# Performance work log

Measured on AMD Instinct MI355X. Metric: run time of the kernel, lower is better.

Reference implementation:

```python
import jax, jax.numpy as jnp
import numpy as np

D = 512
H = 8
HD = D // H
EPS = 1e-6


def layer_norm(x, a, b):
    # torch: std is unbiased (ddof=1); note division by (std + eps), not sqrt(var+eps)
    mean = x.mean(-1, keepdims=True)
    std = jnp.sqrt(x.var(-1, ddof=1, keepdims=True))
    return a * (x - mean) / (std + EPS) + b


def setup_inputs() -> dict:
    key = jax.random.key(0)
    ks = jax.random.split(key, 8)
    x = jax.random.normal(ks[0], (4, 2048, D), dtype=jnp.float32)
    s = 0.02
    return {
        "x": x,
        "ln1_a": jnp.ones((D,), jnp.float32),
        "ln1_b": jnp.zeros((D,), jnp.float32),
        "ln2_a": jnp.ones((D,), jnp.float32),
        "ln2_b": jnp.zeros((D,), jnp.float32),
        "wq": jax.random.normal(ks[1], (D, D), jnp.float32) * s,  # [out, in] torch layout
        "wk": jax.random.normal(ks[2], (D, D), jnp.float32) * s,
        "wv": jax.random.normal(ks[3], (D, D), jnp.float32) * s,
        "wo": jax.random.normal(ks[4], (D, D), jnp.float32) * s,
        "w1": jax.random.normal(ks[5], (D, D), jnp.float32) * s,  # MLP hidden == dim
        "b1": jnp.zeros((D,), jnp.float32),
        "w2": jax.random.normal(ks[6], (D, D), jnp.float32) * s,
        "b2": jnp.zeros((D,), jnp.float32),
    }


def reference(x, ln1_a, ln1_b, ln2_a, ln2_b, wq, wk, wv, wo, w1, b1, w2, b2):
    B, S, _ = x.shape
    xn = layer_norm(x, ln1_a, ln1_b)
    # attention (non-causal, dropout=identity in eval)
    q = (xn @ wq.T).reshape(B, S, H, HD)
    k = (xn @ wk.T).reshape(B, S, H, HD)
    v = (xn @ wv.T).reshape(B, S, H, HD)
    scores = jnp.einsum("bshd,bthd->bhst", q, k) / jnp.sqrt(jnp.float32(HD))
    probs = jax.nn.softmax(scores.astype(jnp.float32), axis=-1).astype(q.dtype)
    attn = jnp.einsum("bhst,bthd->bshd", probs, v).reshape(B, S, D)
    h = xn + attn @ wo.T
    # MLP
    hn = layer_norm(h, ln2_a, ln2_b)
    ffn = jax.nn.relu(hn @ w1.T + b1) @ w2.T + b2
    return h + ffn
```

## Files before the change

### kernel.cpp

```cpp
#include <hip/hip_runtime.h>


typedef short s16x8 __attribute__((ext_vector_type(8)));
typedef float f32x4 __attribute__((ext_vector_type(4)));
typedef unsigned short u16;
typedef u16 u16x4 __attribute__((ext_vector_type(4)));

__device__ __forceinline__ u16 f2b(float f) {
  union { float f; unsigned u; } c; c.f = f;
  return (u16)((c.u + 0x7FFFu + ((c.u >> 16) & 1u)) >> 16);
}

__device__ __forceinline__ f32x4 mfma16(s16x8 a, s16x8 b, f32x4 c) {
  return __builtin_amdgcn_mfma_f32_16x16x32_bf16(a, b, c, 0, 0, 0);
}

__device__ __forceinline__ void gload_lds16(const u16* g, u16* l) {
  __builtin_amdgcn_global_load_lds(
      (const __attribute__((address_space(1))) unsigned*)g,
      (__attribute__((address_space(3))) unsigned*)l, 16, 0, 0);
}

__global__ __launch_bounds__(256) void cast_w(
    const float* __restrict__ s0, const float* __restrict__ s1,
    const float* __restrict__ s2, const float* __restrict__ s3,
    const float* __restrict__ s4, const float* __restrict__ s5,
    u16* __restrict__ dst)
{
  int i = blockIdx.x * 256 + threadIdx.x;
  const float* s;
  switch (blockIdx.y) {
    case 0: s = s0; break; case 1: s = s1; break; case 2: s = s2; break;
    case 3: s = s3; break; case 4: s = s4; break; default: s = s5; break;
  }
  float4 v = ((const float4*)s)[i];
  u16x4 o; o.x = f2b(v.x); o.y = f2b(v.y); o.z = f2b(v.z); o.w = f2b(v.w);
  *(u16x4*)(dst + (size_t)blockIdx.y * 262144 + (size_t)i * 4) = o;
}

template<int OF, int OB>
__global__ __launch_bounds__(256) void ln_kernel(
    const float* __restrict__ x, const float* __restrict__ ga,
    const float* __restrict__ gbv, float* __restrict__ yf, u16* __restrict__ yb)
{
  int row = blockIdx.x * 4 + (threadIdx.x >> 6);
  int lane = threadIdx.x & 63;
  size_t base = (size_t)row * 512 + lane * 8;
  const float4* xr = (const float4*)(x + base);
  float4 v0 = xr[0], v1 = xr[1];
  float s  = v0.x + v0.y + v0.z + v0.w + v1.x + v1.y + v1.z + v1.w;
  float ss = v0.x*v0.x + v0.y*v0.y + v0.z*v0.z + v0.w*v0.w
           + v1.x*v1.x + v1.y*v1.y + v1.z*v1.z + v1.w*v1.w;
  #pragma unroll
  for (int m = 1; m < 64; m <<= 1) { s += __shfl_xor(s, m); ss += __shfl_xor(ss, m); }
  float mean = s * (1.0f / 512.0f);
  float var  = fmaxf((ss - 512.0f * mean * mean) * (1.0f / 511.0f), 0.0f);
  float inv  = 1.0f / (sqrtf(var) + 1e-6f);
  const float4* ap = (const float4*)(ga + lane * 8);
  const float4* bp = (const float4*)(gbv + lane * 8);
  float4 a0 = ap[0], a1 = ap[1], b0 = bp[0], b1 = bp[1];
  float4 y0, y1;
  y0.x = (v0.x-mean)*inv*a0.x + b0.x;  y0.y = (v0.y-mean)*inv*a0.y + b0.y;
  y0.z = (v0.z-mean)*inv*a0.z + b0.z;  y0.w = (v0.w-mean)*inv*a0.w + b0.w;
  y1.x = (v1.x-mean)*inv*a1.x + b1.x;  y1.y = (v1.y-mean)*inv*a1.y + b1.y;
  y1.z = (v1.z-mean)*inv*a1.z + b1.z;  y1.w = (v1.w-mean)*inv*a1.w + b1.w;
  if (OF) { float4* o = (float4*)(yf + base); o[0] = y0; o[1] = y1; }
  if (OB) {
    union { s16x8 v; u16 u[8]; } pk;
    pk.u[0]=f2b(y0.x); pk.u[1]=f2b(y0.y); pk.u[2]=f2b(y0.z); pk.u[3]=f2b(y0.w);
    pk.u[4]=f2b(y1.x); pk.u[5]=f2b(y1.y); pk.u[6]=f2b(y1.z); pk.u[7]=f2b(y1.w);
    *(s16x8*)(yb + base) = pk.v;
  }
}

template<int MODE>
__global__ __launch_bounds__(256) void gemm128(
    const u16* __restrict__ A, const u16* __restrict__ W,
    const float* __restrict__ bias, const float* __restrict__ resid,
    float* __restrict__ outf, u16* __restrict__ outb,
    u16* __restrict__ outb2, u16* __restrict__ outb3, float qscale)
{
  __shared__ u16 als[2][128 * 32];
  __shared__ u16 bls[2][128 * 32];
  int t = threadIdx.x, lane = t & 63, w = t >> 6;
  int l15 = lane & 15, g = lane >> 4;
  int wr = w >> 1, wc = w & 1;
  int mbase = blockIdx.x * 128, nbase = blockIdx.y * 128;

  int r0 = t >> 2, cs = (t & 3) ^ ((r0 >> 1) & 3);
  size_t offA0 = (size_t)(mbase + r0) * 512 + cs * 8;
  size_t offA1 = (size_t)(mbase + r0 + 64) * 512 + cs * 8;
  size_t offB0 = (size_t)(nbase + r0) * 512 + cs * 8;
  size_t offB1 = (size_t)(nbase + r0 + 64) * 512 + cs * 8;

  #define GSTAGE(buf, k0) do {                                    \
    gload_lds16(A + (k0) + offA0, &als[buf][(w * 64) * 8]);       \
    gload_lds16(A + (k0) + offA1, &als[buf][(256 + w * 64) * 8]); \
    gload_lds16(W + (k0) + offB0, &bls[buf][(w * 64) * 8]);       \
    gload_lds16(W + (k0) + offB1, &bls[buf][(256 + w * 64) * 8]); \
  } while (0)

  int ar[4], br[4];
  #pragma unroll
  for (int i = 0; i < 4; ++i) {
    int rA = wr * 64 + i * 16 + l15;
    ar[i] = rA * 32 + ((g ^ ((rA >> 1) & 3)) << 3);
    int rB = wc * 64 + i * 16 + l15;
    br[i] = rB * 32 + ((g ^ ((rB >> 1) & 3)) << 3);
  }

  f32x4 zero = {0.0f, 0.0f, 0.0f, 0.0f};
  f32x4 acc[4][4];
  #pragma unroll
  for (int mi = 0; mi < 4; ++mi)
    #pragma unroll
    for (int ni = 0; ni < 4; ++ni) acc[mi][ni] = zero;

  GSTAGE(0, 0);
  __syncthreads();
  int cur = 0;
  for (int kk = 0; kk < 16; ++kk) {
    if (kk < 15) GSTAGE(cur ^ 1, (kk + 1) * 32);
    s16x8 af[4], bfr[4];
    #pragma unroll
    for (int i = 0; i < 4; ++i) {
      af[i]  = *(const s16x8*)&als[cur][ar[i]];
      bfr[i] = *(const s16x8*)&bls[cur][br[i]];
    }
    #pragma unroll
    for (int mi = 0; mi < 4; ++mi)
      #pragma unroll
      for (int ni = 0; ni < 4; ++ni)
        acc[mi][ni] = mfma16(af[mi], bfr[ni], acc[mi][ni]);
    __syncthreads();
    cur ^= 1;
  }
  #undef GSTAGE

  #pragma unroll
  for (int ni = 0; ni < 4; ++ni) {
    int n = nbase + wc * 64 + ni * 16 + l15;
    float bv = (MODE & 1) ? bias[n] : 0.0f;
    #pragma unroll
    for (int mi = 0; mi < 4; ++mi) {
      #pragma unroll
      for (int r = 0; r < 4; ++r) {
        int m = mbase + wr * 64 + mi * 16 + 4 * g + r;
        float v = acc[mi][ni][r] + bv;
        if (MODE & 2) v = fmaxf(v, 0.0f);
        if (MODE & 4) v += resid[(size_t)m * 512 + n];
        if (MODE & 8) outf[(size_t)m * 512 + n] = v;
        if (MODE & 16) outb[(size_t)m * 512 + n] = f2b(v);
        if (MODE & 64) {
          if (nbase < 512) {
            outb[(size_t)m * 512 + n] = f2b(v * qscale);
          } else if (nbase < 1024) {
            outb2[(size_t)m * 512 + (n - 512)] = f2b(v);
          } else {
            int nn = n - 1024;
            int sidx = m & 2047;
            int jj = sidx & 31, lo4 = jj & 15, b5 = jj >> 4;
            int pos = ((lo4 >> 2) << 3) + ((lo4 & 3) << 1) + b5;
            outb3[(size_t)((m >> 11) * 512 + nn) * 2048 + (sidx & ~31) + pos] = f2b(v);
          }
        }
      }
    }
  }
}

__global__ __launch_bounds__(256) void attn_kernel(
    const u16* __restrict__ q, const u16* __restrict__ k,
    const u16* __restrict__ vt, u16* __restrict__ o)
{
  __shared__ u16 kls[2][64 * 64];
  __shared__ u16 vls[2][64 * 64];
  int t = threadIdx.x, lane = t & 63, w = t >> 6;
  int l15 = lane & 15, g = lane >> 4;
  int sw = l15 & 7;
  int lrow = lane >> 3;
  int lchunk = (lane & 7) ^ (lrow & 7);
  int fid = blockIdx.x + 32 * blockIdx.y;
  int xcd = fid & 7, rest = fid >> 3;
  int bh = xcd * 4 + (rest & 3);
  int qt = rest >> 2;
  int bb = bh >> 3, h = bh & 7;
  int qbase = qt * 64 + w * 16;

  const u16* qp = q + (size_t)(bb * 2048 + qbase + l15) * 512 + h * 64 + g * 8;
  s16x8 qf0 = *(const s16x8*)qp;
  s16x8 qf1 = *(const s16x8*)(qp + 32);
  f32x4 zero = {0.0f, 0.0f, 0.0f, 0.0f};
  f32x4 oacc[4] = {zero, zero, zero, zero};
  float lsum = 0.0f;
  const u16* kb0 = k + (size_t)(bb * 2048) * 512 + h * 64;
  const u16* vb0 = vt + (size_t)((bb * 8 + h) * 64) * 2048;

  #define STAGE(nb, tt) do {                                                  \
    int r0 = w * 16 + lrow;                                                   \
    const u16* ks0 = kb0 + (size_t)((tt) * 64 + r0) * 512 + lchunk * 8;       \
    const u16* vs0 = vb0 + (size_t)r0 * 2048 + (tt) * 64 + lchunk * 8;        \
    gload_lds16(ks0, &kls[nb][(w * 16) * 64]);                                \
    gload_lds16(ks0 + (size_t)8 * 512, &kls[nb][(w * 16 + 8) * 64]);          \
    gload_lds16(vs0, &vls[nb][(w * 16) * 64]);                                \
    gload_lds16(vs0 + (size_t)8 * 2048, &vls[nb][(w * 16 + 8) * 64]);         \
  } while (0)

  STAGE(0, 0);
  __syncthreads();
  int cur = 0;

  for (int kt = 0; kt < 32; ++kt) {
    if (kt + 1 < 32) STAGE(cur ^ 1, kt + 1);
    f32x4 s[4];
    #pragma unroll
    for (int kg = 0; kg < 4; ++kg) {
      int rb = (kg * 16 + l15) * 64;
      s16x8 ka = *(const s16x8*)&kls[cur][rb + ((g ^ sw) << 3)];
      s16x8 kc = *(const s16x8*)&kls[cur][rb + (((4 + g) ^ sw) << 3)];
      s[kg] = mfma16(ka, qf0, zero);
      s[kg] = mfma16(kc, qf1, s[kg]);
    }
    union { s16x8 v8; unsigned u32v[4]; } pk[2];
    #pragma unroll
    for (int b2 = 0; b2 < 2; ++b2) {
      #pragma unroll
      for (int r = 0; r < 4; ++r) {
        float p0 = __builtin_amdgcn_exp2f(s[2 * b2][r]);
        float p1 = __builtin_amdgcn_exp2f(s[2 * b2 + 1][r]);
        lsum += p0 + p1;
        union { float f; unsigned u; } a, b;
        a.f = p0; b.f = p1;
        pk[b2].u32v[r] = (a.u >> 16) | (b.u & 0xffff0000u);
      }
    }
    #pragma unroll
    for (int b2 = 0; b2 < 2; ++b2) {
      #pragma unroll
      for (int nf = 0; nf < 4; ++nf) {
        s16x8 vf = *(const s16x8*)
            &vls[cur][(nf * 16 + l15) * 64 + ((((b2 << 2) | g) ^ sw) << 3)];
        oacc[nf] = mfma16(pk[b2].v8, vf, oacc[nf]);
      }
    }
    __syncthreads();
    cur ^= 1;
  }
  #undef STAGE

  lsum += __shfl_xor(lsum, 16);
  lsum += __shfl_xor(lsum, 32);
  float linv = 1.0f / lsum;
  size_t obase = (size_t)(bb * 2048 + qbase + 4 * g) * 512 + h * 64 + l15;
  #pragma unroll
  for (int r = 0; r < 4; ++r) {
    float lr = __shfl(linv, 4 * g + r);
    #pragma unroll
    for (int nf = 0; nf < 4; ++nf)
      o[obase + (size_t)r * 512 + nf * 16] = f2b(oacc[nf][r] * lr);
  }
}

extern "C" void kernel_launch(void* const* d_in, const int* in_sizes, int n_in,
                              void* d_out, int out_size, void* d_ws, size_t ws_size,
                              hipStream_t stream)
{
  const float* x     = (const float*)d_in[0];
  const float* ln1_a = (const float*)d_in[1];
  const float* ln1_b = (const float*)d_in[2];
  const float* ln2_a = (const float*)d_in[3];
  const float* ln2_b = (const float*)d_in[4];
  const float* wq = (const float*)d_in[5];
  const float* wk = (const float*)d_in[6];
  const float* wv = (const float*)d_in[7];
  const float* wo = (const float*)d_in[8];
  const float* w1 = (const float*)d_in[9];
  const float* b1 = (const float*)d_in[10];
  const float* w2 = (const float*)d_in[11];
  const float* b2 = (const float*)d_in[12];

  char* ws = (char*)d_ws;
  float* xn_f = (float*)(ws + (size_t)0);
  float* h_f  = (float*)(ws + ((size_t)16 << 20));
  u16* xn_b = (u16*)(ws + ((size_t)32 << 20));
  u16* q_b  = (u16*)(ws + ((size_t)40 << 20));
  u16* k_b  = (u16*)(ws + ((size_t)48 << 20));
  u16* vt_b = (u16*)(ws + ((size_t)56 << 20));
  u16* at_b = (u16*)(ws + ((size_t)64 << 20));
  u16* wb   = (u16*)(ws + ((size_t)72 << 20));
  u16 *wob = wb + 3*262144, *w1b = wb + 4 * 262144, *w2b = wb + 5 * 262144;
  u16* hn_b = q_b;
  u16* f_b  = at_b;

  dim3 blk(256);
  cast_w<<<dim3(256, 6), blk, 0, stream>>>(wq, wk, wv, wo, w1, w2, wb);
  ln_kernel<1, 1><<<dim3(2048), blk, 0, stream>>>(x, ln1_a, ln1_b, xn_f, xn_b);
  gemm128<64><<<dim3(64, 12), blk, 0, stream>>>(
      xn_b, wb, nullptr, nullptr, nullptr, q_b, k_b, vt_b, 0.18033688f);
  attn_kernel<<<dim3(32, 32), blk, 0, stream>>>(q_b, k_b, vt_b, at_b);
  gemm128<4 | 8><<<dim3(64, 4), blk, 0, stream>>>(
      at_b, wob, nullptr, xn_f, h_f, nullptr, nullptr, nullptr, 0.0f);
  ln_kernel<0, 1><<<dim3(2048), blk, 0, stream>>>(h_f, ln2_a, ln2_b, nullptr, hn_b);
  gemm128<1 | 2 | 16><<<dim3(64, 4), blk, 0, stream>>>(
      hn_b, w1b, b1, nullptr, nullptr, f_b, nullptr, nullptr, 0.0f);
  gemm128<1 | 4 | 8><<<dim3(64, 4), blk, 0, stream>>>(
      f_b, w2b, b2, h_f, (float*)d_out, nullptr, nullptr, nullptr, 0.0f);
}
```

Measured before the change: 141.9 us.

## Process two query sub-tiles per wave in attention to reuse K/V fragments

Each wave now handles 32 query rows instead of 16, so each block covers 128 queries and the grid is halved. Every K and V fragment read from LDS now feeds two MFMAs, which halves LDS traffic and global K/V staging per query. The bf16 packing also switches to a single v_perm instruction. In exchange the kernel uses more registers and launches fewer blocks (512), which may lower occupancy.

```diff
diff --git a/kernel.cpp b/kernel.cpp
--- a/kernel.cpp
+++ b/kernel.cpp
@@ -185,14 +185,20 @@
   int bh = xcd * 4 + (rest & 3);
   int qt = rest >> 2;
   int bb = bh >> 3, h = bh & 7;
-  int qbase = qt * 64 + w * 16;
+  int qbase = qt * 128 + w * 32;
 
   const u16* qp = q + (size_t)(bb * 2048 + qbase + l15) * 512 + h * 64 + g * 8;
-  s16x8 qf0 = *(const s16x8*)qp;
-  s16x8 qf1 = *(const s16x8*)(qp + 32);
+  s16x8 qf0a = *(const s16x8*)qp;
+  s16x8 qf1a = *(const s16x8*)(qp + 32);
+  s16x8 qf0b = *(const s16x8*)(qp + 16 * 512);
+  s16x8 qf1b = *(const s16x8*)(qp + 16 * 512 + 32);
   f32x4 zero = {0.0f, 0.0f, 0.0f, 0.0f};
-  f32x4 oacc[4] = {zero, zero, zero, zero};
-  float lsum = 0.0f;
+  f32x4 oacc[2][4];
+  #pragma unroll
+  for (int qg = 0; qg < 2; ++qg)
+    #pragma unroll
+    for (int nf = 0; nf < 4; ++nf) oacc[qg][nf] = zero;
+  float lsum[2] = {0.0f, 0.0f};
   const u16* kb0 = k + (size_t)(bb * 2048) * 512 + h * 64;
   const u16* vb0 = vt + (size_t)((bb * 8 + h) * 64) * 2048;
 
@@ -212,26 +218,31 @@
 
   for (int kt = 0; kt < 32; ++kt) {
     if (kt + 1 < 32) STAGE(cur ^ 1, kt + 1);
-    f32x4 s[4];
+    f32x4 s[2][4];
     #pragma unroll
     for (int kg = 0; kg < 4; ++kg) {
       int rb = (kg * 16 + l15) * 64;
       s16x8 ka = *(const s16x8*)&kls[cur][rb + ((g ^ sw) << 3)];
       s16x8 kc = *(const s16x8*)&kls[cur][rb + (((4 + g) ^ sw) << 3)];
-      s[kg] = mfma16(ka, qf0, zero);
-      s[kg] = mfma16(kc, qf1, s[kg]);
-    }
-    union { s16x8 v8; unsigned u32v[4]; } pk[2];
-    #pragma unroll
-    for (int b2 = 0; b2 < 2; ++b2) {
-      #pragma unroll
-      for (int r = 0; r < 4; ++r) {
-        float p0 = __builtin_amdgcn_exp2f(s[2 * b2][r]);
-        float p1 = __builtin_amdgcn_exp2f(s[2 * b2 + 1][r]);
-        lsum += p0 + p1;
-        union { float f; unsigned u; } a, b;
-        a.f = p0; b.f = p1;
-        pk[b2].u32v[r] = (a.u >> 16) | (b.u & 0xffff0000u);
+      s[0][kg] = mfma16(ka, qf0a, zero);
+      s[0][kg] = mfma16(kc, qf1a, s[0][kg]);
+      s[1][kg] = mfma16(ka, qf0b, zero);
+      s[1][kg] = mfma16(kc, qf1b, s[1][kg]);
+    }
+    union { s16x8 v8; unsigned u32v[4]; } pk[2][2];
+    #pragma unroll
+    for (int qg = 0; qg < 2; ++qg) {
+      #pragma unroll
+      for (int b2 = 0; b2 < 2; ++b2) {
+        #pragma unroll
+        for (int r = 0; r < 4; ++r) {
+          float p0 = __builtin_amdgcn_exp2f(s[qg][2 * b2][r]);
+          float p1 = __builtin_amdgcn_exp2f(s[qg][2 * b2 + 1][r]);
+          lsum[qg] += p0 + p1;
+          union { float f; unsigned u; } a, b;
+          a.f = p0; b.f = p1;
+          pk[qg][b2].u32v[r] = __builtin_amdgcn_perm(b.u, a.u, 0x07060302u);
+        }
       }
     }
     #pragma unroll
@@ -240,7 +251,8 @@
       for (int nf = 0; nf < 4; ++nf) {
         s16x8 vf = *(const s16x8*)
             &vls[cur][(nf * 16 + l15) * 64 + ((((b2 << 2) | g) ^ sw) << 3)];
-        oacc[nf] = mfma16(pk[b2].v8, vf, oacc[nf]);
+        oacc[0][nf] = mfma16(pk[0][b2].v8, vf, oacc[0][nf]);
+        oacc[1][nf] = mfma16(pk[1][b2].v8, vf, oacc[1][nf]);
       }
     }
     __syncthreads();
@@ -248,16 +260,21 @@
   }
   #undef STAGE
 
-  lsum += __shfl_xor(lsum, 16);
-  lsum += __shfl_xor(lsum, 32);
-  float linv = 1.0f / lsum;
-  size_t obase = (size_t)(bb * 2048 + qbase + 4 * g) * 512 + h * 64 + l15;
-  #pragma unroll
-  for (int r = 0; r < 4; ++r) {
-    float lr = __shfl(linv, 4 * g + r);
-    #pragma unroll
-    for (int nf = 0; nf < 4; ++nf)
-      o[obase + (size_t)r * 512 + nf * 16] = f2b(oacc[nf][r] * lr);
+  #pragma unroll
+  for (int qg = 0; qg < 2; ++qg) {
+    float ls = lsum[qg];
+    ls += __shfl_xor(ls, 16);
+    ls += __shfl_xor(ls, 32);
+    float linv = 1.0f / ls;
+    size_t obase = (size_t)(bb * 2048 + qbase + qg * 16 + 4 * g) * 512
+                 + h * 64 + l15;
+    #pragma unroll
+    for (int r = 0; r < 4; ++r) {
+      float lr = __shfl(linv, 4 * g + r);
+      #pragma unroll
+      for (int nf = 0; nf < 4; ++nf)
+        o[obase + (size_t)r * 512 + nf * 16] = f2b(oacc[qg][nf][r] * lr);
+    }
   }
 }
 
@@ -297,7 +314,7 @@
   ln_kernel<1, 1><<<dim3(2048), blk, 0, stream>>>(x, ln1_a, ln1_b, xn_f, xn_b);
   gemm128<64><<<dim3(64, 12), blk, 0, stream>>>(
       xn_b, wb, nullptr, nullptr, nullptr, q_b, k_b, vt_b, 0.18033688f);
-  attn_kernel<<<dim3(32, 32), blk, 0, stream>>>(q_b, k_b, vt_b, at_b);
+  attn_kernel<<<dim3(32, 16), blk, 0, stream>>>(q_b, k_b, vt_b, at_b);
   gemm128<4 | 8><<<dim3(64, 4), blk, 0, stream>>>(
       at_b, wob, nullptr, xn_f, h_f, nullptr, nullptr, nullptr, 0.0f);
   ln_kernel<0, 1><<<dim3(2048), blk, 0, stream>>>(h_f, ln2_a, ln2_b, nullptr, hn_b);
```

Result: faster. 137.8 us (-2.9%).
